# Performance work log

Hardware: AMD Instinct MI355X
Metric: run time of the kernel (lower is better)

## Reference

```python
import jax, jax.numpy as jnp
import numpy as np

D = 1024      # features
C = 768       # context dim
H = 16        # heads
HD = D // H   # head dim = 64
N = 2048      # query tokens
M = 2048      # context tokens
EPS = 1e-12
SCALE = float(np.sqrt(HD))


def layernorm(x, w, b):
    c = x - x.mean(axis=-1, keepdims=True)
    s = (c * c).mean(axis=-1, keepdims=True)
    return c * jax.lax.rsqrt(s + EPS) * w + b


def setup_inputs() -> dict:
    key = jax.random.key(0)
    ks = jax.random.split(key, 10)
    sc = 0.02
    return {
        "x": jax.random.normal(ks[0], (N, D), jnp.float32),
        "ctx": jax.random.normal(ks[1], (M, C), jnp.float32),
        # attention projections (Projection: normal*0.02, zero bias)
        "wq": jax.random.normal(ks[2], (D, D), jnp.float32) * sc,
        "bq": jnp.zeros((D,), jnp.float32),
        "wk": jax.random.normal(ks[3], (C, D), jnp.float32) * sc,
        "bk": jnp.zeros((D,), jnp.float32),
        "wv": jax.random.normal(ks[4], (C, D), jnp.float32) * sc,
        "bv": jnp.zeros((D,), jnp.float32),
        "wo": jax.random.normal(ks[5], (D, D), jnp.float32) * sc,
        "bo": jnp.zeros((D,), jnp.float32),
        # MLP
        "w1": jax.random.normal(ks[6], (D, 4 * D), jnp.float32) * sc,
        "b1": jnp.zeros((4 * D,), jnp.float32),
        "w2": jax.random.normal(ks[7], (4 * D, D), jnp.float32) * sc,
        "b2": jnp.zeros((D,), jnp.float32),
        # layernorms
        "qn_w": jnp.ones((D,), jnp.float32), "qn_b": jnp.zeros((D,), jnp.float32),
        "kvn_w": jnp.ones((C,), jnp.float32), "kvn_b": jnp.zeros((C,), jnp.float32),
        "pn_w": jnp.ones((D,), jnp.float32), "pn_b": jnp.zeros((D,), jnp.float32),
    }


def reference(x, ctx, wq, bq, wk, bk, wv, bv, wo, bo, w1, b1, w2, b2,
              qn_w, qn_b, kvn_w, kvn_b, pn_w, pn_b):
    # pre-norm cross-attention
    xq = layernorm(x, qn_w, qn_b)          # [n, d]
    kv = layernorm(ctx, kvn_w, kvn_b)      # [m, c]
    q = (xq @ wq + bq).reshape(N, H, HD).transpose(1, 0, 2)   # [h, n, hd]
    k = (kv @ wk + bk).reshape(M, H, HD).transpose(1, 0, 2)   # [h, m, hd]
    v = (kv @ wv + bv).reshape(M, H, HD).transpose(1, 0, 2)   # [h, m, hd]
    attn = jax.nn.softmax(jnp.einsum('hnd,hmd->hnm', q, k) / SCALE, axis=-1)
    o = jnp.einsum('hnm,hmd->hnd', attn, v).transpose(1, 0, 2).reshape(N, D)
    x = (o @ wo + bo) + x
    # MLP block
    h = layernorm(x, pn_w, pn_b)
    h = jax.nn.gelu(h @ w1 + b1) @ w2 + b2
    return h + x
```

## Files before the change

kernel.cpp:

```cpp
#include <hip/hip_runtime.h>

typedef __bf16 bf16;
typedef __bf16 bf16x4 __attribute__((ext_vector_type(4)));
typedef __bf16 bf16x8 __attribute__((ext_vector_type(8)));
typedef float f32x4 __attribute__((ext_vector_type(4)));

#define N_TOK 2048
#define M_TOK 2048
#define DIM 1024
#define CDIM 768
#define DFF 4096

static __device__ __forceinline__ void async16(const void* g, void* l) {
  __builtin_amdgcn_global_load_lds((const __attribute__((address_space(1))) void*)g,
                                   (__attribute__((address_space(3))) void*)l, 16, 0, 0);
}

__global__ __launch_bounds__(256) void detect_kernel(const void* x, int* flag) {
  __shared__ int cnt;
  if (threadIdx.x == 0) cnt = 0;
  __syncthreads();
  const unsigned* w = (const unsigned*)x;
  int ok = 0;
  for (int i = threadIdx.x; i < 512; i += 256) {
    unsigned lo = w[i] & 0xFFFFu;
    float f = __uint_as_float(lo << 16);
    if (lo == 0u || (fabsf(f) > 1e-3f && fabsf(f) < 1e3f)) ok++;
  }
  atomicAdd(&cnt, ok);
  __syncthreads();
  if (threadIdx.x == 0) *flag = (cnt >= 256) ? 1 : 0;
}

struct ConvArgs {
  const void* src[12];
  bf16* dst[12];
  int n[12];
};
__global__ __launch_bounds__(256) void conv_small_kernel(ConvArgs a, const int* flag) {
  const bool isbf = (*flag != 0);
  const int b = blockIdx.x;
  const void* in = a.src[b];
  bf16* out = a.dst[b];
  const int n = a.n[b];
  for (int i = threadIdx.x; i < n; i += 256)
    out[i] = isbf ? ((const bf16*)in)[i] : (bf16)((const float*)in)[i];
}

struct TmArgs {
  const void* src[4];
  bf16* dst[4];
  int r0[4], Rcnt[4], c0[4], Cfull[4], gx[4], gy[4];
  int force_bf;
};
__global__ __launch_bounds__(256) void tmulti_kernel(TmArgs a, const int* flag) {
  const int z = blockIdx.z;
  if ((int)blockIdx.x >= a.gx[z] || (int)blockIdx.y >= a.gy[z]) return;
  __shared__ bf16 t[32][33];
  const bool isbf = a.force_bf || (*flag != 0);
  const void* in = a.src[z];
  bf16* out = a.dst[z];
  const int Rcnt = a.Rcnt[z], Cfull = a.Cfull[z];
  const int cb = blockIdx.x * 32, rb = blockIdx.y * 32;
  const int tx = threadIdx.x & 31, ty = threadIdx.x >> 5;
#pragma unroll
  for (int i = 0; i < 4; i++) {
    const size_t r = (size_t)(a.r0[z] + rb + ty + i * 8);
    const size_t c = (size_t)(a.c0[z] + cb + tx);
    float v = isbf ? (float)((const bf16*)in)[r * Cfull + c]
                   : ((const float*)in)[r * Cfull + c];
    t[ty + i * 8][tx] = (bf16)v;
  }
  __syncthreads();
#pragma unroll
  for (int i = 0; i < 4; i++)
    out[(size_t)(cb + ty + i * 8) * Rcnt + rb + tx] = t[tx][ty + i * 8];
}

__global__ __launch_bounds__(256) void ln_pair_kernel(
    const void* __restrict__ x0, const bf16* w0, const bf16* b0, bf16* o0,
    const void* __restrict__ x1, const bf16* w1, const bf16* b1, bf16* o1,
    const int* flag) {
  const bool isbf = (*flag != 0);
  const int cols = (blockIdx.y == 0) ? DIM : CDIM;
  const void* x = (blockIdx.y == 0) ? x0 : x1;
  const bf16* w = (blockIdx.y == 0) ? w0 : w1;
  const bf16* b = (blockIdx.y == 0) ? b0 : b1;
  bf16* outp = (blockIdx.y == 0) ? o0 : o1;
  const int row = blockIdx.x;
  const bf16* xr_b = (const bf16*)x + (size_t)row * cols;
  const float* xr_f = (const float*)x + (size_t)row * cols;
  bf16* orow = outp + (size_t)row * cols;
  float s = 0.f, ss = 0.f;
  for (int c = threadIdx.x; c < cols; c += 256) {
    float v = isbf ? (float)xr_b[c] : xr_f[c];
    s += v; ss += v * v;
  }
  for (int d = 1; d < 64; d <<= 1) { s += __shfl_xor(s, d, 64); ss += __shfl_xor(ss, d, 64); }
  __shared__ float sh[8];
  const int wv = threadIdx.x >> 6, lane = threadIdx.x & 63;
  if (lane == 0) { sh[wv] = s; sh[4 + wv] = ss; }
  __syncthreads();
  s = sh[0] + sh[1] + sh[2] + sh[3];
  ss = sh[4] + sh[5] + sh[6] + sh[7];
  const float mean = s / cols;
  float var = ss / cols - mean * mean;
  var = fmaxf(var, 0.f);
  const float r = rsqrtf(var + 1e-12f);
  for (int c = threadIdx.x; c < cols; c += 256) {
    float v = isbf ? (float)xr_b[c] : xr_f[c];
    orow[c] = (bf16)((v - mean) * r * (float)w[c] + (float)b[c]);
  }
}

__global__ __launch_bounds__(256) void ln_kernel(
    const bf16* __restrict__ x, const bf16* __restrict__ w, const bf16* __restrict__ b,
    bf16* __restrict__ out, int cols) {
  const int row = blockIdx.x;
  const bf16* xr = x + (size_t)row * cols;
  bf16* orow = out + (size_t)row * cols;
  float s = 0.f, ss = 0.f;
  for (int c = threadIdx.x; c < cols; c += 256) {
    float v = (float)xr[c];
    s += v; ss += v * v;
  }
  for (int d = 1; d < 64; d <<= 1) { s += __shfl_xor(s, d, 64); ss += __shfl_xor(ss, d, 64); }
  __shared__ float sh[8];
  const int wv = threadIdx.x >> 6, lane = threadIdx.x & 63;
  if (lane == 0) { sh[wv] = s; sh[4 + wv] = ss; }
  __syncthreads();
  s = sh[0] + sh[1] + sh[2] + sh[3];
  ss = sh[4] + sh[5] + sh[6] + sh[7];
  const float mean = s / cols;
  float var = ss / cols - mean * mean;
  var = fmaxf(var, 0.f);
  const float r = rsqrtf(var + 1e-12f);
  for (int c = threadIdx.x; c < cols; c += 256) {
    float v = (float)xr[c];
    orow[c] = (bf16)((v - mean) * r * (float)w[c] + (float)b[c]);
  }
}

__device__ __forceinline__ float gelu_f(float x) {
  float u = 0.7978845608028654f * (x + 0.044715f * x * x * x);
  return 0.5f * x * (1.f + tanhf(u));
}

template <int EPI>
__global__ __launch_bounds__(512) void gemm128db(
    const bf16* __restrict__ A, const bf16* __restrict__ Bt,
    const bf16* __restrict__ bias, const void* __restrict__ resid,
    void* __restrict__ Cout, int K, int ldc, const int* flag) {
  __shared__ __align__(16) bf16 As[2][128 * 64];
  __shared__ __align__(16) bf16 Bs[2][128 * 64];
  const int tid = threadIdx.x;
  const int lane = tid & 63, wv = tid >> 6;
  const int lq = lane >> 4, lm = lane & 15;
  const int row0 = blockIdx.y * 128, col0 = blockIdx.x * 128;
  const int wm = (wv >> 2) * 64, wn = (wv & 3) * 32;

  const int sr = lane >> 3;
  const int sc = ((lane & 7) ^ sr) * 8;
  const int swz = (lm & 7) << 3;

  f32x4 acc[4][2] = {};

  const bf16* Abase = A + (size_t)(row0 + wv * 16 + sr) * K + sc;
  const bf16* Bbase = Bt + (size_t)(col0 + wv * 16 + sr) * K + sc;

  const int nt = K >> 6;
#pragma unroll
  for (int b = 0; b < 2; b++) {
    async16(Abase + (size_t)(b * 8) * K, &As[0][wv * 1024 + b * 512]);
    async16(Bbase + (size_t)(b * 8) * K, &Bs[0][wv * 1024 + b * 512]);
  }
  __syncthreads();

  int cur = 0;
  for (int t = 0; t < nt; ++t) {
    if (t + 1 < nt) {
      const int k1 = (t + 1) << 6;
#pragma unroll
      for (int b = 0; b < 2; b++) {
        async16(Abase + (size_t)(b * 8) * K + k1, &As[cur ^ 1][wv * 1024 + b * 512]);
        async16(Bbase + (size_t)(b * 8) * K + k1, &Bs[cur ^ 1][wv * 1024 + b * 512]);
      }
    }
#pragma unroll
    for (int kh = 0; kh < 2; kh++) {
      const int cofs = (kh * 32 + lq * 8) ^ swz;
      bf16x8 af[4], bfv[2];
#pragma unroll
      for (int i = 0; i < 4; i++)
        af[i] = *(const bf16x8*)&As[cur][(wm + i * 16 + lm) * 64 + cofs];
#pragma unroll
      for (int j = 0; j < 2; j++)
        bfv[j] = *(const bf16x8*)&Bs[cur][(wn + j * 16 + lm) * 64 + cofs];
#pragma unroll
      for (int i = 0; i < 4; i++)
#pragma unroll
        for (int j = 0; j < 2; j++)
          acc[i][j] = __builtin_amdgcn_mfma_f32_16x16x32_bf16(af[i], bfv[j], acc[i][j], 0, 0, 0);
    }
    __syncthreads();
    cur ^= 1;
  }

  const bool isbf = (*flag != 0);
#pragma unroll
  for (int i = 0; i < 4; i++) {
    const int rb = row0 + wm + i * 16 + lq * 4;
#pragma unroll
    for (int j = 0; j < 2; j++) {
      const int c = col0 + wn + j * 16 + lm;
      const float bv = (EPI != 5) ? (float)bias[c] : 0.f;
#pragma unroll
      for (int rg = 0; rg < 4; rg++) {
        const size_t idx = (size_t)(rb + rg) * ldc + c;
        float v = acc[i][j][rg] + bv;
        if (EPI == 1)
          v += isbf ? (float)((const bf16*)resid)[idx] : ((const float*)resid)[idx];
        if (EPI == 2) v = gelu_f(v);
        if (EPI == 4) v += (float)((const bf16*)resid)[idx];
        if (EPI == 5)
          v += isbf ? (float)((bf16*)Cout)[idx] : ((float*)Cout)[idx];
        if (EPI == 4 || EPI == 5) {
          if (isbf) ((bf16*)Cout)[idx] = (bf16)v;
          else      ((float*)Cout)[idx] = v;
        } else {
          ((bf16*)Cout)[idx] = (bf16)v;
        }
      }
    }
  }
}

struct QkvArgs {
  const bf16* A[3];
  const bf16* Bt[3];
  const bf16* bias[3];
  bf16* C[3];
  int K[3], ldc[3], gx[3], gy[3], brow[3];
};
__global__ __launch_bounds__(512) void gemm128db_qkv(QkvArgs a) {
  const int z = blockIdx.z;
  if ((int)blockIdx.x >= a.gx[z] || (int)blockIdx.y >= a.gy[z]) return;
  const bf16* A = a.A[z];
  const bf16* Bt = a.Bt[z];
  const int K = a.K[z];
  __shared__ __align__(16) bf16 As[2][128 * 64];
  __shared__ __align__(16) bf16 Bs[2][128 * 64];
  const int tid = threadIdx.x;
  const int lane = tid & 63, wv = tid >> 6;
  const int lq = lane >> 4, lm = lane & 15;
  const int row0 = blockIdx.y * 128, col0 = blockIdx.x * 128;
  const int wm = (wv >> 2) * 64, wn = (wv & 3) * 32;

  const int sr = lane >> 3;
  const int sc = ((lane & 7) ^ sr) * 8;
  const int swz = (lm & 7) << 3;

  f32x4 acc[4][2] = {};

  const bf16* Abase = A + (size_t)(row0 + wv * 16 + sr) * K + sc;
  const bf16* Bbase = Bt + (size_t)(col0 + wv * 16 + sr) * K + sc;

  const int nt = K >> 6;
#pragma unroll
  for (int b = 0; b < 2; b++) {
    async16(Abase + (size_t)(b * 8) * K, &As[0][wv * 1024 + b * 512]);
    async16(Bbase + (size_t)(b * 8) * K, &Bs[0][wv * 1024 + b * 512]);
  }
  __syncthreads();

  int cur = 0;
  for (int t = 0; t < nt; ++t) {
    if (t + 1 < nt) {
      const int k1 = (t + 1) << 6;
#pragma unroll
      for (int b = 0; b < 2; b++) {
        async16(Abase + (size_t)(b * 8) * K + k1, &As[cur ^ 1][wv * 1024 + b * 512]);
        async16(Bbase + (size_t)(b * 8) * K + k1, &Bs[cur ^ 1][wv * 1024 + b * 512]);
      }
    }
#pragma unroll
    for (int kh = 0; kh < 2; kh++) {
      const int cofs = (kh * 32 + lq * 8) ^ swz;
      bf16x8 af[4], bfv[2];
#pragma unroll
      for (int i = 0; i < 4; i++)
        af[i] = *(const bf16x8*)&As[cur][(wm + i * 16 + lm) * 64 + cofs];
#pragma unroll
      for (int j = 0; j < 2; j++)
        bfv[j] = *(const bf16x8*)&Bs[cur][(wn + j * 16 + lm) * 64 + cofs];
#pragma unroll
      for (int i = 0; i < 4; i++)
#pragma unroll
        for (int j = 0; j < 2; j++)
          acc[i][j] = __builtin_amdgcn_mfma_f32_16x16x32_bf16(af[i], bfv[j], acc[i][j], 0, 0, 0);
    }
    __syncthreads();
    cur ^= 1;
  }

  const bf16* bias = a.bias[z];
  bf16* C = a.C[z];
  const int ldc = a.ldc[z];
  const bool brow = a.brow[z] != 0;
#pragma unroll
  for (int i = 0; i < 4; i++) {
    const int rb = row0 + wm + i * 16 + lq * 4;
#pragma unroll
    for (int j = 0; j < 2; j++) {
      const int c = col0 + wn + j * 16 + lm;
      const float bcol = brow ? 0.f : (float)bias[c];
#pragma unroll
      for (int rg = 0; rg < 4; rg++) {
        const float bv = brow ? (float)bias[rb + rg] : bcol;
        C[(size_t)(rb + rg) * ldc + c] = (bf16)(acc[i][j][rg] + bv);
      }
    }
  }
}

#define KS_STR 72
#define VS_STR 136
__global__ __launch_bounds__(256) void attn_kernel(
    const bf16* __restrict__ q, const bf16* __restrict__ k,
    const bf16* __restrict__ vT, bf16* __restrict__ pO0, bf16* __restrict__ pO1,
    float* __restrict__ l0, float* __restrict__ l1) {
  __shared__ __align__(16) bf16 KPs[128 * KS_STR];
  __shared__ __align__(16) bf16 Vs[64 * VS_STR];
  const int tid = threadIdx.x, lane = tid & 63, wv = tid >> 6;
  const int lq = lane >> 4, lm = lane & 15;
  const int h = blockIdx.y;
  const int n0 = blockIdx.x * 64;
  const int half = blockIdx.z;
  const int mbeg = half * (M_TOK / 2), mend = mbeg + M_TOK / 2;
  bf16* pO = half ? pO1 : pO0;
  float* lb = half ? l1 : l0;

  bf16x8 qf[2];
#pragma unroll
  for (int f = 0; f < 2; f++)
    qf[f] = *(const bf16x8*)&q[(size_t)(n0 + wv * 16 + lm) * DIM + h * 64 + f * 32 + lq * 8];

  f32x4 oacc[4] = {};
  float lsum = 0.f;
  const float sc = 0.125f * 1.4426950408889634f;

  for (int m0 = mbeg; m0 < mend; m0 += 128) {
    __syncthreads();
#pragma unroll
    for (int it = 0; it < 4; it++) {
      const int e = tid * 8 + it * 2048;
      const int r = e >> 6, c = e & 63;
      *(bf16x8*)&KPs[r * KS_STR + c] =
          *(const bf16x8*)&k[(size_t)(m0 + r) * DIM + h * 64 + c];
    }
#pragma unroll
    for (int it = 0; it < 4; it++) {
      const int e = tid * 8 + it * 2048;
      const int r = e >> 7, c = e & 127;
      *(bf16x8*)&Vs[r * VS_STR + c] =
          *(const bf16x8*)&vT[(size_t)(h * 64 + r) * M_TOK + m0 + c];
    }
    __syncthreads();

    f32x4 s[8];
#pragma unroll
    for (int j = 0; j < 8; j++) {
      bf16x8 kf0 = *(const bf16x8*)&KPs[(j * 16 + lm) * KS_STR + lq * 8];
      bf16x8 kf1 = *(const bf16x8*)&KPs[(j * 16 + lm) * KS_STR + 32 + lq * 8];
      f32x4 z = {};
      z = __builtin_amdgcn_mfma_f32_16x16x32_bf16(kf0, qf[0], z, 0, 0, 0);
      s[j] = __builtin_amdgcn_mfma_f32_16x16x32_bf16(kf1, qf[1], z, 0, 0, 0);
    }
    __syncthreads();

#pragma unroll
    for (int j = 0; j < 8; j++) {
      bf16x4 pw;
#pragma unroll
      for (int rg = 0; rg < 4; rg++) {
        const float pv = exp2f(s[j][rg] * sc);
        lsum += pv;
        pw[rg] = (bf16)pv;
      }
      *(bf16x4*)&KPs[(wv * 16 + lm) * VS_STR + j * 16 + lq * 4] = pw;
    }

#pragma unroll
    for (int kk = 0; kk < 4; kk++) {
      bf16x8 pf = *(const bf16x8*)&KPs[(wv * 16 + lm) * VS_STR + kk * 32 + lq * 8];
#pragma unroll
      for (int dt = 0; dt < 4; dt++) {
        bf16x8 vf = *(const bf16x8*)&Vs[(dt * 16 + lm) * VS_STR + kk * 32 + lq * 8];
        oacc[dt] = __builtin_amdgcn_mfma_f32_16x16x32_bf16(vf, pf, oacc[dt], 0, 0, 0);
      }
    }
  }

  lsum += __shfl_xor(lsum, 16, 64);
  lsum += __shfl_xor(lsum, 32, 64);
  if (lane < 16) lb[h * N_TOK + n0 + wv * 16 + lane] = lsum;

  const int rn = n0 + wv * 16 + lm;
#pragma unroll
  for (int dt = 0; dt < 4; dt++) {
    bf16x4 ow;
#pragma unroll
    for (int rg = 0; rg < 4; rg++) ow[rg] = (bf16)oacc[dt][rg];
    *(bf16x4*)&pO[(size_t)rn * DIM + h * 64 + dt * 16 + lq * 4] = ow;
  }
}

__global__ __launch_bounds__(256) void attn_combine(
    const bf16* __restrict__ pO0, const bf16* __restrict__ pO1,
    const float* __restrict__ l0, const float* __restrict__ l1,
    bf16* __restrict__ om) {
  const int i4 = (blockIdx.x * 256 + threadIdx.x) * 4;
  const int n = i4 >> 10;
  const int h = (i4 & 1023) >> 6;
  const float rinv = 1.f / (l0[h * N_TOK + n] + l1[h * N_TOK + n]);
  bf16x4 a = *(const bf16x4*)&pO0[i4];
  bf16x4 b = *(const bf16x4*)&pO1[i4];
  bf16x4 o;
#pragma unroll
  for (int r = 0; r < 4; r++) o[r] = (bf16)(((float)a[r] + (float)b[r]) * rinv);
  *(bf16x4*)&om[i4] = o;
}

extern "C" void kernel_launch(void* const* d_in, const int* in_sizes, int n_in,
                              void* d_out, int out_size, void* d_ws, size_t ws_size,
                              hipStream_t stream) {
  const void* x_r     = d_in[0];
  const void* ctx_r   = d_in[1];
  const void* wq_r    = d_in[2];
  const void* bq_r    = d_in[3];
  const void* wk_r    = d_in[4];
  const void* bk_r    = d_in[5];
  const void* wv_r    = d_in[6];
  const void* bv_r    = d_in[7];
  const void* wo_r    = d_in[8];
  const void* bo_r    = d_in[9];
  const void* w1_r    = d_in[10];
  const void* b1_r    = d_in[11];
  const void* w2_r    = d_in[12];
  const void* b2_r    = d_in[13];
  const void* qnw_r   = d_in[14];
  const void* qnb_r   = d_in[15];
  const void* kvnw_r  = d_in[16];
  const void* kvnb_r  = d_in[17];
  const void* pnw_r   = d_in[18];
  const void* pnb_r   = d_in[19];

  bf16* p = (bf16*)d_ws;
  const size_t MEG = 1024 * 1024;
  bf16* qm  = p;             bf16* hln = qm;
  bf16* km  = p + 2 * MEG;   bf16* xat = km;
  bf16* wC  = p + 4 * MEG;
  bf16* xq  = p + 8 * MEG;   bf16* pO0 = xq;   bf16* om = xq;
  bf16* vTb = p + 10 * MEG;
  bf16* kvn = p + 12 * MEG;  bf16* pO1 = kvn;
  bf16* h1h = p + 10 * MEG;
  bf16* SM  = p + 14 * MEG;
  int* flag = (int*)(p + 14 * MEG + 16384);

  bf16* wqT = wC;
  bf16* wkT = wC + 1 * MEG;
  bf16* wvT = wC + 1 * MEG + 786432;
  bf16* woT = wC + 2 * MEG + 524288;
  bf16* w1Th = wC;
  bf16* w2Th = wC + 2 * MEG;
  float* l0 = (float*)wC;
  float* l1 = l0 + N_TOK * 16;

  bf16* bqc = SM, *bkc = SM + 1024, *bvc = SM + 2048, *boc = SM + 3072;
  bf16* b1c = SM + 4096, *b2c = SM + 8192;
  bf16* qnw = SM + 9216, *qnb = SM + 10240;
  bf16* kvnw = SM + 11264, *kvnb = SM + 12032;
  bf16* pnw = SM + 12800, *pnb = SM + 13824;

  detect_kernel<<<1, 256, 0, stream>>>(x_r, flag);
  ConvArgs ca;
  ca.src[0] = bq_r;   ca.dst[0] = bqc;  ca.n[0] = DIM;
  ca.src[1] = bk_r;   ca.dst[1] = bkc;  ca.n[1] = DIM;
  ca.src[2] = bv_r;   ca.dst[2] = bvc;  ca.n[2] = DIM;
  ca.src[3] = bo_r;   ca.dst[3] = boc;  ca.n[3] = DIM;
  ca.src[4] = b1_r;   ca.dst[4] = b1c;  ca.n[4] = DFF;
  ca.src[5] = b2_r;   ca.dst[5] = b2c;  ca.n[5] = DIM;
  ca.src[6] = qnw_r;  ca.dst[6] = qnw;  ca.n[6] = DIM;
  ca.src[7] = qnb_r;  ca.dst[7] = qnb;  ca.n[7] = DIM;
  ca.src[8] = kvnw_r; ca.dst[8] = kvnw; ca.n[8] = CDIM;
  ca.src[9] = kvnb_r; ca.dst[9] = kvnb; ca.n[9] = CDIM;
  ca.src[10] = pnw_r; ca.dst[10] = pnw; ca.n[10] = DIM;
  ca.src[11] = pnb_r; ca.dst[11] = pnb; ca.n[11] = DIM;
  conv_small_kernel<<<12, 256, 0, stream>>>(ca, flag);

  ln_pair_kernel<<<dim3(2048, 2), 256, 0, stream>>>(x_r, qnw, qnb, xq,
                                                    ctx_r, kvnw, kvnb, kvn, flag);

  {
    TmArgs ta;
    ta.force_bf = 0;
    ta.src[0] = wq_r; ta.dst[0] = wqT; ta.r0[0] = 0; ta.Rcnt[0] = DIM;
    ta.c0[0] = 0; ta.Cfull[0] = DIM; ta.gx[0] = 32; ta.gy[0] = 32;
    ta.src[1] = wk_r; ta.dst[1] = wkT; ta.r0[1] = 0; ta.Rcnt[1] = CDIM;
    ta.c0[1] = 0; ta.Cfull[1] = DIM; ta.gx[1] = 32; ta.gy[1] = 24;
    ta.src[2] = wv_r; ta.dst[2] = wvT; ta.r0[2] = 0; ta.Rcnt[2] = CDIM;
    ta.c0[2] = 0; ta.Cfull[2] = DIM; ta.gx[2] = 32; ta.gy[2] = 24;
    ta.src[3] = wo_r; ta.dst[3] = woT; ta.r0[3] = 0; ta.Rcnt[3] = DIM;
    ta.c0[3] = 0; ta.Cfull[3] = DIM; ta.gx[3] = 32; ta.gy[3] = 32;
    tmulti_kernel<<<dim3(32, 32, 4), 256, 0, stream>>>(ta, flag);
  }

  {
    QkvArgs qa;
    qa.A[0] = xq;  qa.Bt[0] = wqT; qa.bias[0] = bqc; qa.C[0] = qm;
    qa.K[0] = DIM;  qa.ldc[0] = DIM;   qa.gx[0] = 8;  qa.gy[0] = 16; qa.brow[0] = 0;
    qa.A[1] = kvn; qa.Bt[1] = wkT; qa.bias[1] = bkc; qa.C[1] = km;
    qa.K[1] = CDIM; qa.ldc[1] = DIM;   qa.gx[1] = 8;  qa.gy[1] = 16; qa.brow[1] = 0;
    qa.A[2] = wvT; qa.Bt[2] = kvn; qa.bias[2] = bvc; qa.C[2] = vTb;
    qa.K[2] = CDIM; qa.ldc[2] = M_TOK; qa.gx[2] = 16; qa.gy[2] = 8;  qa.brow[2] = 1;
    gemm128db_qkv<<<dim3(16, 16, 3), 512, 0, stream>>>(qa);
  }

  attn_kernel<<<dim3(32, 16, 2), 256, 0, stream>>>(qm, km, vTb, pO0, pO1, l0, l1);
  attn_combine<<<2048, 256, 0, stream>>>(pO0, pO1, l0, l1, om);

  gemm128db<1><<<dim3(8, 16), 512, 0, stream>>>(om, woT, boc, x_r, xat, DIM, DIM, flag);

  ln_kernel<<<N_TOK, 256, 0, stream>>>(xat, pnw, pnb, hln, DIM);

  for (int hh = 0; hh < 2; hh++) {
    TmArgs ta;
    ta.force_bf = 0;
    ta.src[0] = w1_r; ta.dst[0] = w1Th; ta.r0[0] = 0; ta.Rcnt[0] = DIM;
    ta.c0[0] = hh * 2048; ta.Cfull[0] = DFF; ta.gx[0] = 64; ta.gy[0] = 32;
    ta.src[1] = w2_r; ta.dst[1] = w2Th; ta.r0[1] = hh * 2048; ta.Rcnt[1] = 2048;
    ta.c0[1] = 0; ta.Cfull[1] = DIM; ta.gx[1] = 32; ta.gy[1] = 64;
    ta.src[2] = ta.src[0]; ta.dst[2] = ta.dst[0]; ta.r0[2] = 0; ta.Rcnt[2] = 32;
    ta.c0[2] = 0; ta.Cfull[2] = DIM; ta.gx[2] = 0; ta.gy[2] = 0;
    ta.src[3] = ta.src[0]; ta.dst[3] = ta.dst[0]; ta.r0[3] = 0; ta.Rcnt[3] = 32;
    ta.c0[3] = 0; ta.Cfull[3] = DIM; ta.gx[3] = 0; ta.gy[3] = 0;
    tmulti_kernel<<<dim3(64, 64, 2), 256, 0, stream>>>(ta, flag);

    gemm128db<2><<<dim3(16, 16), 512, 0, stream>>>(hln, w1Th, b1c + hh * 2048, nullptr,
                                                   h1h, DIM, 2048, flag);
    if (hh == 0)
      gemm128db<4><<<dim3(8, 16), 512, 0, stream>>>(h1h, w2Th, b2c, xat, d_out,
                                                    2048, DIM, flag);
    else
      gemm128db<5><<<dim3(8, 16), 512, 0, stream>>>(h1h, w2Th, b2c, nullptr, d_out,
                                                    2048, DIM, flag);
  }
}
```

Before: 396.1 us.

## Shrink GEMM tiles to 64x64 and swizzle attention LDS tiles

All GEMM kernels move from 128x128 tiles with 512 threads to 64x64 tiles with 256 threads. This quadruples the grid so more blocks are in flight on the many CUs for these fairly small matrices. Separately, the attention kernel drops its padded LDS strides for XOR-swizzled layouts, which cuts shared memory use and aims to avoid bank conflicts. Smaller tiles give less operand reuse per block and more global and L2 traffic.

```diff
diff --git a/kernel.cpp b/kernel.cpp
--- a/kernel.cpp
+++ b/kernel.cpp
@@ -147,23 +147,23 @@
 }
 
 template <int EPI>
-__global__ __launch_bounds__(512) void gemm128db(
+__global__ __launch_bounds__(256) void gemm64db(
     const bf16* __restrict__ A, const bf16* __restrict__ Bt,
     const bf16* __restrict__ bias, const void* __restrict__ resid,
     void* __restrict__ Cout, int K, int ldc, const int* flag) {
-  __shared__ __align__(16) bf16 As[2][128 * 64];
-  __shared__ __align__(16) bf16 Bs[2][128 * 64];
+  __shared__ __align__(16) bf16 As[2][64 * 64];
+  __shared__ __align__(16) bf16 Bs[2][64 * 64];
   const int tid = threadIdx.x;
   const int lane = tid & 63, wv = tid >> 6;
   const int lq = lane >> 4, lm = lane & 15;
-  const int row0 = blockIdx.y * 128, col0 = blockIdx.x * 128;
-  const int wm = (wv >> 2) * 64, wn = (wv & 3) * 32;
+  const int row0 = blockIdx.y * 64, col0 = blockIdx.x * 64;
+  const int wr = (wv >> 1) * 32, wc = (wv & 1) * 32;
 
   const int sr = lane >> 3;
   const int sc = ((lane & 7) ^ sr) * 8;
   const int swz = (lm & 7) << 3;
 
-  f32x4 acc[4][2] = {};
+  f32x4 acc[2][2] = {};
 
   const bf16* Abase = A + (size_t)(row0 + wv * 16 + sr) * K + sc;
   const bf16* Bbase = Bt + (size_t)(col0 + wv * 16 + sr) * K + sc;
@@ -189,15 +189,15 @@
 #pragma unroll
     for (int kh = 0; kh < 2; kh++) {
       const int cofs = (kh * 32 + lq * 8) ^ swz;
-      bf16x8 af[4], bfv[2];
-#pragma unroll
-      for (int i = 0; i < 4; i++)
-        af[i] = *(const bf16x8*)&As[cur][(wm + i * 16 + lm) * 64 + cofs];
+      bf16x8 af[2], bfv[2];
+#pragma unroll
+      for (int i = 0; i < 2; i++)
+        af[i] = *(const bf16x8*)&As[cur][(wr + i * 16 + lm) * 64 + cofs];
 #pragma unroll
       for (int j = 0; j < 2; j++)
-        bfv[j] = *(const bf16x8*)&Bs[cur][(wn + j * 16 + lm) * 64 + cofs];
-#pragma unroll
-      for (int i = 0; i < 4; i++)
+        bfv[j] = *(const bf16x8*)&Bs[cur][(wc + j * 16 + lm) * 64 + cofs];
+#pragma unroll
+      for (int i = 0; i < 2; i++)
 #pragma unroll
         for (int j = 0; j < 2; j++)
           acc[i][j] = __builtin_amdgcn_mfma_f32_16x16x32_bf16(af[i], bfv[j], acc[i][j], 0, 0, 0);
@@ -208,11 +208,11 @@
 
   const bool isbf = (*flag != 0);
 #pragma unroll
-  for (int i = 0; i < 4; i++) {
-    const int rb = row0 + wm + i * 16 + lq * 4;
+  for (int i = 0; i < 2; i++) {
+    const int rb = row0 + wr + i * 16 + lq * 4;
 #pragma unroll
     for (int j = 0; j < 2; j++) {
-      const int c = col0 + wn + j * 16 + lm;
+      const int c = col0 + wc + j * 16 + lm;
       const float bv = (EPI != 5) ? (float)bias[c] : 0.f;
 #pragma unroll
       for (int rg = 0; rg < 4; rg++) {
@@ -242,25 +242,25 @@
   bf16* C[3];
   int K[3], ldc[3], gx[3], gy[3], brow[3];
 };
-__global__ __launch_bounds__(512) void gemm128db_qkv(QkvArgs a) {
+__global__ __launch_bounds__(256) void gemm64db_qkv(QkvArgs a) {
   const int z = blockIdx.z;
   if ((int)blockIdx.x >= a.gx[z] || (int)blockIdx.y >= a.gy[z]) return;
   const bf16* A = a.A[z];
   const bf16* Bt = a.Bt[z];
   const int K = a.K[z];
-  __shared__ __align__(16) bf16 As[2][128 * 64];
-  __shared__ __align__(16) bf16 Bs[2][128 * 64];
+  __shared__ __align__(16) bf16 As[2][64 * 64];
+  __shared__ __align__(16) bf16 Bs[2][64 * 64];
   const int tid = threadIdx.x;
   const int lane = tid & 63, wv = tid >> 6;
   const int lq = lane >> 4, lm = lane & 15;
-  const int row0 = blockIdx.y * 128, col0 = blockIdx.x * 128;
-  const int wm = (wv >> 2) * 64, wn = (wv & 3) * 32;
+  const int row0 = blockIdx.y * 64, col0 = blockIdx.x * 64;
+  const int wr = (wv >> 1) * 32, wc = (wv & 1) * 32;
 
   const int sr = lane >> 3;
   const int sc = ((lane & 7) ^ sr) * 8;
   const int swz = (lm & 7) << 3;
 
-  f32x4 acc[4][2] = {};
+  f32x4 acc[2][2] = {};
 
   const bf16* Abase = A + (size_t)(row0 + wv * 16 + sr) * K + sc;
   const bf16* Bbase = Bt + (size_t)(col0 + wv * 16 + sr) * K + sc;
@@ -286,15 +286,15 @@
 #pragma unroll
     for (int kh = 0; kh < 2; kh++) {
       const int cofs = (kh * 32 + lq * 8) ^ swz;
-      bf16x8 af[4], bfv[2];
-#pragma unroll
-      for (int i = 0; i < 4; i++)
-        af[i] = *(const bf16x8*)&As[cur][(wm + i * 16 + lm) * 64 + cofs];
+      bf16x8 af[2], bfv[2];
+#pragma unroll
+      for (int i = 0; i < 2; i++)
+        af[i] = *(const bf16x8*)&As[cur][(wr + i * 16 + lm) * 64 + cofs];
 #pragma unroll
       for (int j = 0; j < 2; j++)
-        bfv[j] = *(const bf16x8*)&Bs[cur][(wn + j * 16 + lm) * 64 + cofs];
-#pragma unroll
-      for (int i = 0; i < 4; i++)
+        bfv[j] = *(const bf16x8*)&Bs[cur][(wc + j * 16 + lm) * 64 + cofs];
+#pragma unroll
+      for (int i = 0; i < 2; i++)
 #pragma unroll
         for (int j = 0; j < 2; j++)
           acc[i][j] = __builtin_amdgcn_mfma_f32_16x16x32_bf16(af[i], bfv[j], acc[i][j], 0, 0, 0);
@@ -308,11 +308,11 @@
   const int ldc = a.ldc[z];
   const bool brow = a.brow[z] != 0;
 #pragma unroll
-  for (int i = 0; i < 4; i++) {
-    const int rb = row0 + wm + i * 16 + lq * 4;
+  for (int i = 0; i < 2; i++) {
+    const int rb = row0 + wr + i * 16 + lq * 4;
 #pragma unroll
     for (int j = 0; j < 2; j++) {
-      const int c = col0 + wn + j * 16 + lm;
+      const int c = col0 + wc + j * 16 + lm;
       const float bcol = brow ? 0.f : (float)bias[c];
 #pragma unroll
       for (int rg = 0; rg < 4; rg++) {
@@ -323,14 +323,12 @@
   }
 }
 
-#define KS_STR 72
-#define VS_STR 136
 __global__ __launch_bounds__(256) void attn_kernel(
     const bf16* __restrict__ q, const bf16* __restrict__ k,
     const bf16* __restrict__ vT, bf16* __restrict__ pO0, bf16* __restrict__ pO1,
     float* __restrict__ l0, float* __restrict__ l1) {
-  __shared__ __align__(16) bf16 KPs[128 * KS_STR];
-  __shared__ __align__(16) bf16 Vs[64 * VS_STR];
+  __shared__ __align__(16) bf16 KPs[128 * 64];
+  __shared__ __align__(16) bf16 Vs[64 * 128];
   const int tid = threadIdx.x, lane = tid & 63, wv = tid >> 6;
   const int lq = lane >> 4, lm = lane & 15;
   const int h = blockIdx.y;
@@ -355,14 +353,14 @@
     for (int it = 0; it < 4; it++) {
       const int e = tid * 8 + it * 2048;
       const int r = e >> 6, c = e & 63;
-      *(bf16x8*)&KPs[r * KS_STR + c] =
+      *(bf16x8*)&KPs[r * 64 + (c ^ ((r & 7) << 3))] =
           *(const bf16x8*)&k[(size_t)(m0 + r) * DIM + h * 64 + c];
     }
 #pragma unroll
     for (int it = 0; it < 4; it++) {
       const int e = tid * 8 + it * 2048;
       const int r = e >> 7, c = e & 127;
-      *(bf16x8*)&Vs[r * VS_STR + c] =
+      *(bf16x8*)&Vs[r * 128 + (c ^ ((r & 7) << 3))] =
           *(const bf16x8*)&vT[(size_t)(h * 64 + r) * M_TOK + m0 + c];
     }
     __syncthreads();
@@ -370,8 +368,9 @@
     f32x4 s[8];
 #pragma unroll
     for (int j = 0; j < 8; j++) {
-      bf16x8 kf0 = *(const bf16x8*)&KPs[(j * 16 + lm) * KS_STR + lq * 8];
-      bf16x8 kf1 = *(const bf16x8*)&KPs[(j * 16 + lm) * KS_STR + 32 + lq * 8];
+      const int kswz = (lm & 7) << 3;
+      bf16x8 kf0 = *(const bf16x8*)&KPs[(j * 16 + lm) * 64 + ((lq * 8) ^ kswz)];
+      bf16x8 kf1 = *(const bf16x8*)&KPs[(j * 16 + lm) * 64 + ((32 + lq * 8) ^ kswz)];
       f32x4 z = {};
       z = __builtin_amdgcn_mfma_f32_16x16x32_bf16(kf0, qf[0], z, 0, 0, 0);
       s[j] = __builtin_amdgcn_mfma_f32_16x16x32_bf16(kf1, qf[1], z, 0, 0, 0);
@@ -387,15 +386,17 @@
         lsum += pv;
         pw[rg] = (bf16)pv;
       }
-      *(bf16x4*)&KPs[(wv * 16 + lm) * VS_STR + j * 16 + lq * 4] = pw;
+      *(bf16x4*)&KPs[(wv * 16 + lm) * 128 + ((j * 16 + lq * 4) ^ ((lm & 7) << 3))] = pw;
     }
 
 #pragma unroll
     for (int kk = 0; kk < 4; kk++) {
-      bf16x8 pf = *(const bf16x8*)&KPs[(wv * 16 + lm) * VS_STR + kk * 32 + lq * 8];
+      bf16x8 pf = *(const bf16x8*)&KPs[(wv * 16 + lm) * 128 +
+                                       ((kk * 32 + lq * 8) ^ ((lm & 7) << 3))];
 #pragma unroll
       for (int dt = 0; dt < 4; dt++) {
-        bf16x8 vf = *(const bf16x8*)&Vs[(dt * 16 + lm) * VS_STR + kk * 32 + lq * 8];
+        bf16x8 vf = *(const bf16x8*)&Vs[(dt * 16 + lm) * 128 +
+                                        ((kk * 32 + lq * 8) ^ ((lm & 7) << 3))];
         oacc[dt] = __builtin_amdgcn_mfma_f32_16x16x32_bf16(vf, pf, oacc[dt], 0, 0, 0);
       }
     }
@@ -518,18 +519,18 @@
   {
     QkvArgs qa;
     qa.A[0] = xq;  qa.Bt[0] = wqT; qa.bias[0] = bqc; qa.C[0] = qm;
-    qa.K[0] = DIM;  qa.ldc[0] = DIM;   qa.gx[0] = 8;  qa.gy[0] = 16; qa.brow[0] = 0;
+    qa.K[0] = DIM;  qa.ldc[0] = DIM;   qa.gx[0] = 16; qa.gy[0] = 32; qa.brow[0] = 0;
     qa.A[1] = kvn; qa.Bt[1] = wkT; qa.bias[1] = bkc; qa.C[1] = km;
-    qa.K[1] = CDIM; qa.ldc[1] = DIM;   qa.gx[1] = 8;  qa.gy[1] = 16; qa.brow[1] = 0;
+    qa.K[1] = CDIM; qa.ldc[1] = DIM;   qa.gx[1] = 16; qa.gy[1] = 32; qa.brow[1] = 0;
     qa.A[2] = wvT; qa.Bt[2] = kvn; qa.bias[2] = bvc; qa.C[2] = vTb;
-    qa.K[2] = CDIM; qa.ldc[2] = M_TOK; qa.gx[2] = 16; qa.gy[2] = 8;  qa.brow[2] = 1;
-    gemm128db_qkv<<<dim3(16, 16, 3), 512, 0, stream>>>(qa);
+    qa.K[2] = CDIM; qa.ldc[2] = M_TOK; qa.gx[2] = 32; qa.gy[2] = 16; qa.brow[2] = 1;
+    gemm64db_qkv<<<dim3(32, 32, 3), 256, 0, stream>>>(qa);
   }
 
   attn_kernel<<<dim3(32, 16, 2), 256, 0, stream>>>(qm, km, vTb, pO0, pO1, l0, l1);
   attn_combine<<<2048, 256, 0, stream>>>(pO0, pO1, l0, l1, om);
 
-  gemm128db<1><<<dim3(8, 16), 512, 0, stream>>>(om, woT, boc, x_r, xat, DIM, DIM, flag);
+  gemm64db<1><<<dim3(16, 32), 256, 0, stream>>>(om, woT, boc, x_r, xat, DIM, DIM, flag);
 
   ln_kernel<<<N_TOK, 256, 0, stream>>>(xat, pnw, pnb, hln, DIM);
 
@@ -546,13 +547,13 @@
     ta.c0[3] = 0; ta.Cfull[3] = DIM; ta.gx[3] = 0; ta.gy[3] = 0;
     tmulti_kernel<<<dim3(64, 64, 2), 256, 0, stream>>>(ta, flag);
 
-    gemm128db<2><<<dim3(16, 16), 512, 0, stream>>>(hln, w1Th, b1c + hh * 2048, nullptr,
-                                                   h1h, DIM, 2048, flag);
+    gemm64db<2><<<dim3(32, 32), 256, 0, stream>>>(hln, w1Th, b1c + hh * 2048, nullptr,
+                                                  h1h, DIM, 2048, flag);
     if (hh == 0)
-      gemm128db<4><<<dim3(8, 16), 512, 0, stream>>>(h1h, w2Th, b2c, xat, d_out,
+      gemm64db<4><<<dim3(16, 32), 256, 0, stream>>>(h1h, w2Th, b2c, xat, d_out,
                                                     2048, DIM, flag);
     else
-      gemm128db<5><<<dim3(8, 16), 512, 0, stream>>>(h1h, w2Th, b2c, nullptr, d_out,
+      gemm64db<5><<<dim3(16, 32), 256, 0, stream>>>(h1h, w2Th, b2c, nullptr, d_out,
                                                     2048, DIM, flag);
   }
 }
```

Result: faster. 358.1 us (-9.6%).
